# Optimization experiments

Measured on AMD Instinct MI355X. Metric: run time of the kernel, lower is better.

## Reference

```python
import jax, jax.numpy as jnp
import numpy as np

D_MODEL = 1024
NUM_HEADS = 16
D_HEAD = D_MODEL // NUM_HEADS
B, T = 2, 2048


def setup_inputs() -> dict:
    key = jax.random.key(0)
    kx, kq, kk, kv, ko = jax.random.split(key, 5)
    # xavier_uniform bound for square (D,D) linear weights
    bound = float(np.sqrt(6.0 / (D_MODEL + D_MODEL)))
    uni = lambda k: jax.random.uniform(k, (D_MODEL, D_MODEL), jnp.float32, -bound, bound)
    return {
        "x": jax.random.normal(kx, (B, T, D_MODEL), jnp.float32),
        "Wq": uni(kq),
        "Wk": uni(kk),
        "Wv": uni(kv),
        "Wo": uni(ko),
    }


def _split_heads(x):
    # (B, T, D) -> (B, H, T, d_head)
    b, t, _ = x.shape
    return x.reshape(b, t, NUM_HEADS, D_HEAD).transpose(0, 2, 1, 3)


def _exclusive_output_mod(Y, V):
    dt = V.dtype
    tiny = jnp.asarray(jnp.finfo(dt).tiny, dt)
    eps = jnp.asarray(jnp.finfo(dt).eps, dt)
    v_sq = jnp.sum(V * V, axis=-1, keepdims=True)
    y_dot_v = jnp.sum(Y * V, axis=-1, keepdims=True)
    scale = jnp.where(v_sq > 0, y_dot_v / jnp.maximum(v_sq, tiny), jnp.zeros_like(y_dot_v))
    Z = Y - scale * V
    residual_norm = jnp.linalg.norm(Z, axis=-1, keepdims=True)
    reference_norm = jnp.maximum(
        jnp.linalg.norm(Y, axis=-1, keepdims=True),
        jnp.linalg.norm(V, axis=-1, keepdims=True),
    )
    cleanup_tol = eps * Z.shape[-1] * reference_norm
    return jnp.where((v_sq > 0) & (residual_norm <= cleanup_tol), jnp.zeros_like(Z), Z)


def reference(x, Wq, Wk, Wv, Wo):
    Q = _split_heads(x @ Wq.T)  # (B,H,T,dh)
    K = _split_heads(x @ Wk.T)
    V = _split_heads(x @ Wv.T)
    sm_scale = 1.0 / np.sqrt(D_HEAD)
    scores = jnp.einsum("bhqd,bhkd->bhqk", Q, K) * sm_scale
    P = jax.nn.softmax(scores, axis=-1)
    Y = jnp.einsum("bhqk,bhkd->bhqd", P, V)
    Z = _exclusive_output_mod(Y, V)
    # merge heads: (B,H,T,dh) -> (B,T,D)
    Zm = Z.transpose(0, 2, 1, 3).reshape(x.shape[0], x.shape[1], D_MODEL)
    return Zm @ Wo.T
```

## Files before the change

### kernel.cpp

```cpp
#include <hip/hip_runtime.h>
#include <math.h>

#define DM   1024
#define TTOK 2048
#define NTOK 4096

typedef __bf16 bf16x8 __attribute__((ext_vector_type(8)));
typedef __bf16 bf16x4 __attribute__((ext_vector_type(4)));
typedef float  f32x4  __attribute__((ext_vector_type(4)));
typedef float  f32x16 __attribute__((ext_vector_type(16)));

#define QSCALE 0.18033688011112042f

#if defined(__has_builtin)
#if __has_builtin(__builtin_amdgcn_exp2f)
#define EXP2F(x) __builtin_amdgcn_exp2f(x)
#endif
#endif
#ifndef EXP2F
#define EXP2F(x) exp2f(x)
#endif

#define GLDS16(g, l) __builtin_amdgcn_global_load_lds( \
    (__attribute__((address_space(1))) void*)(g),      \
    (__attribute__((address_space(3))) void*)(l), 16, 0, 0)

__global__ __launch_bounds__(256)
void cvt_all(const float* __restrict__ x,  const float* __restrict__ Wq,
             const float* __restrict__ Wk, const float* __restrict__ Wv,
             const float* __restrict__ Wo, __bf16* __restrict__ dst) {
    size_t g = ((size_t)blockIdx.x * 256 + threadIdx.x) * 8;
    const float* s;
    size_t off;
    const size_t NX = (size_t)NTOK * DM;
    if (g < NX) { s = x; off = g; }
    else {
        size_t gg = g - NX;
        int w = (int)(gg >> 20);
        off = gg & ((1u << 20) - 1);
        s = (w == 0) ? Wq : (w == 1) ? Wk : (w == 2) ? Wv : Wo;
    }
    float4 a = *(const float4*)(s + off);
    float4 b = *(const float4*)(s + off + 4);
    bf16x8 v;
    v[0] = (__bf16)a.x; v[1] = (__bf16)a.y; v[2] = (__bf16)a.z; v[3] = (__bf16)a.w;
    v[4] = (__bf16)b.x; v[5] = (__bf16)b.y; v[6] = (__bf16)b.z; v[7] = (__bf16)b.w;
    *(bf16x8*)(dst + g) = v;
}

#define LSTR 136
#define DBUF 8192

template<int MODE>
__global__ __launch_bounds__(256)
void gemm_bf16(const __bf16* __restrict__ X,
               const __bf16* __restrict__ W0, const __bf16* __restrict__ W1,
               const __bf16* __restrict__ W2,
               __bf16* __restrict__ Oq, __bf16* __restrict__ Ok,
               __bf16* __restrict__ Ovt, float* __restrict__ Of)
{
    const int z = (MODE == 0) ? blockIdx.z : 3;
    const __bf16 *A, *B;
    int m0, n0;
    if (MODE == 0 && z < 2) {
        A = z ? W1 : W0; B = X;
        m0 = blockIdx.y * 128; n0 = blockIdx.x * 128;
    } else if (MODE == 0) {
        A = X; B = W2;
        m0 = blockIdx.x * 128; n0 = blockIdx.y * 128;
    } else {
        A = X; B = W0;
        int f = blockIdx.x + 8 * blockIdx.y;
        int c = f & 7, i = f >> 3;
        m0 = (4 * c + (i & 3)) * 128;
        n0 = (i >> 2) * 128;
    }

    __shared__ __attribute__((aligned(16))) __bf16 smem[128 * LSTR];

    const int tid  = threadIdx.x;
    const int lane = tid & 63;
    const int wave = tid >> 6;
    const int wm = wave & 1, wn = wave >> 1;
    const int col = lane & 15, quad = lane >> 4;

    const __bf16* Ag = A + (size_t)(m0 + (tid >> 2)) * DM + (tid & 3) * 8;
    const __bf16* Bg = B + (size_t)(n0 + (tid >> 2)) * DM + (tid & 3) * 8;
    __bf16* lA = smem + tid * 8;
    __bf16* lB = smem + 4096 + tid * 8;

    f32x4 acc[4][4];
#pragma unroll
    for (int i = 0; i < 4; ++i)
#pragma unroll
        for (int j = 0; j < 4; ++j)
#pragma unroll
            for (int r = 0; r < 4; ++r) acc[i][j][r] = 0.0f;

    GLDS16(Ag,                   lA);
    GLDS16(Ag + (size_t)64 * DM, lA + 2048);
    GLDS16(Bg,                   lB);
    GLDS16(Bg + (size_t)64 * DM, lB + 2048);
    __syncthreads();

    const int nk = DM / 32;
    for (int t = 0; t < nk; ++t) {
        const int cur = (t & 1) * DBUF;
        const int nxt = DBUF - cur;

        if (t + 1 < nk) {
            const int k1 = (t + 1) * 32;
            GLDS16(Ag + k1,                   lA + nxt);
            GLDS16(Ag + (size_t)64 * DM + k1, lA + nxt + 2048);
            GLDS16(Bg + k1,                   lB + nxt);
            GLDS16(Bg + (size_t)64 * DM + k1, lB + nxt + 2048);
        }

        const __bf16* Asr = smem + cur;
        const __bf16* Bsr = smem + cur + 4096;
        bf16x8 af[4], bfr[4];
#pragma unroll
        for (int i = 0; i < 4; ++i)
            af[i] = *(const bf16x8*)&Asr[(wm * 64 + i * 16 + col) * 32 + quad * 8];
#pragma unroll
        for (int j = 0; j < 4; ++j)
            bfr[j] = *(const bf16x8*)&Bsr[(wn * 64 + j * 16 + col) * 32 + quad * 8];
#pragma unroll
        for (int i = 0; i < 4; ++i)
#pragma unroll
            for (int j = 0; j < 4; ++j)
                acc[i][j] = __builtin_amdgcn_mfma_f32_16x16x32_bf16(af[i], bfr[j], acc[i][j], 0, 0, 0);

        __syncthreads();
    }

    if (MODE == 1) {
#pragma unroll
        for (int i = 0; i < 4; ++i)
#pragma unroll
            for (int j = 0; j < 4; ++j) {
                const int mb = m0 + wm * 64 + i * 16 + quad * 4;
                const int n  = n0 + wn * 64 + j * 16 + col;
#pragma unroll
                for (int r = 0; r < 4; ++r)
                    Of[(size_t)(mb + r) * DM + n] = acc[i][j][r];
            }
        return;
    }

    const float sc = (z == 0) ? QSCALE : 1.0f;
#pragma unroll
    for (int i = 0; i < 4; ++i)
#pragma unroll
        for (int j = 0; j < 4; ++j) {
            const int ml = wm * 64 + i * 16 + quad * 4;
            const int nl = wn * 64 + j * 16 + col;
            bf16x4 pk;
#pragma unroll
            for (int r = 0; r < 4; ++r) pk[r] = (__bf16)(acc[i][j][r] * sc);
            *(bf16x4*)&smem[nl * LSTR + ml] = pk;
        }
    __syncthreads();

#pragma unroll
    for (int it = 0; it < 8; ++it) {
        int c   = tid + 256 * it;
        int row = c >> 4;
        int ch  = (c & 15) * 8;
        bf16x8 v = *(const bf16x8*)&smem[row * LSTR + ch];
        if (z < 2) {
            int t  = n0 + row;
            int b  = t >> 11; t &= 2047;
            int hd = m0 + ch;
            int h  = hd >> 6, d = hd & 63;
            *(bf16x8*)&((z ? Ok : Oq)[(((size_t)(b * 16 + h)) * TTOK + t) * 64 + d]) = v;
        } else {
            int hd = n0 + row;
            int h  = hd >> 6, d = hd & 63;
            int t  = m0 + ch;
            int b  = t >> 11; t &= 2047;
            *(bf16x8*)&Ovt[(((size_t)(b * 16 + h)) * 64 + d) * TTOK + t] = v;
        }
    }
}

__global__ __launch_bounds__(256)
void attn_mfma(const __bf16* __restrict__ Qg, const __bf16* __restrict__ Kg,
               const __bf16* __restrict__ Vtg, __bf16* __restrict__ Zm)
{
    const int bh = blockIdx.y;
    const int q0 = blockIdx.x * 128;
    const size_t base = (size_t)bh * TTOK * 64;

    __shared__ __attribute__((aligned(16))) __bf16 Ks[2][64 * 72];
    __shared__ __attribute__((aligned(16))) __bf16 Vs[2][64 * 72];
    __shared__ __attribute__((aligned(16))) __bf16 Ps[128 * 72];

    const int tid  = threadIdx.x;
    const int lane = tid & 63, wave = tid >> 6;
    const int c32  = lane & 31, h32 = lane >> 5;

    bf16x8 qf[4];
    const __bf16* qrow = Qg + base + (size_t)(q0 + wave * 32 + c32) * 64 + h32 * 8;
#pragma unroll
    for (int st = 0; st < 4; ++st)
        qf[st] = *(const bf16x8*)(qrow + st * 16);

    f32x16 O[2];
#pragma unroll
    for (int r = 0; r < 16; ++r) { O[0][r] = 0.0f; O[1][r] = 0.0f; }
    float lsum = 0.0f;

    const int rs = tid >> 2, soff = (tid & 3) * 16;

    bf16x8 kr0 = *(const bf16x8*)(Kg  + base + (size_t)rs * 64 + soff);
    bf16x8 kr1 = *(const bf16x8*)(Kg  + base + (size_t)rs * 64 + soff + 8);
    bf16x8 vr0 = *(const bf16x8*)(Vtg + base + (size_t)rs * TTOK + soff);
    bf16x8 vr1 = *(const bf16x8*)(Vtg + base + (size_t)rs * TTOK + soff + 8);
    *(bf16x8*)&Ks[0][rs * 72 + soff]     = kr0;
    *(bf16x8*)&Ks[0][rs * 72 + soff + 8] = kr1;
    *(bf16x8*)&Vs[0][rs * 72 + soff]     = vr0;
    *(bf16x8*)&Vs[0][rs * 72 + soff + 8] = vr1;
    {
        const __bf16* kp = Kg  + base + (size_t)(64 + rs) * 64 + soff;
        const __bf16* vp = Vtg + base + (size_t)rs * TTOK + 64 + soff;
        kr0 = *(const bf16x8*)(kp); kr1 = *(const bf16x8*)(kp + 8);
        vr0 = *(const bf16x8*)(vp); vr1 = *(const bf16x8*)(vp + 8);
    }
    __syncthreads();

    const int kb_tgt = (q0 >> 6) + (wave >> 1);
    const int qo     = (wave & 1) * 32 + c32;
    float vq[2][16];

    for (int kb = 0; kb < TTOK / 64; ++kb) {
        const int cur = kb & 1;
        const __bf16* Kc = Ks[cur];
        const __bf16* Vc = Vs[cur];

        f32x16 s0, s1;
#pragma unroll
        for (int r = 0; r < 16; ++r) { s0[r] = 0.0f; s1[r] = 0.0f; }
#pragma unroll
        for (int st = 0; st < 4; ++st) {
            bf16x8 a0 = *(const bf16x8*)&Kc[(c32)      * 72 + h32 * 8 + st * 16];
            bf16x8 a1 = *(const bf16x8*)&Kc[(32 + c32) * 72 + h32 * 8 + st * 16];
            s0 = __builtin_amdgcn_mfma_f32_32x32x16_bf16(a0, qf[st], s0, 0, 0, 0);
            s1 = __builtin_amdgcn_mfma_f32_32x32x16_bf16(a1, qf[st], s1, 0, 0, 0);
        }

#pragma unroll
        for (int kb2 = 0; kb2 < 2; ++kb2) {
#pragma unroll
            for (int g = 0; g < 4; ++g) {
                float p0 = EXP2F(kb2 ? s1[4 * g + 0] : s0[4 * g + 0]);
                float p1 = EXP2F(kb2 ? s1[4 * g + 1] : s0[4 * g + 1]);
                float p2 = EXP2F(kb2 ? s1[4 * g + 2] : s0[4 * g + 2]);
                float p3 = EXP2F(kb2 ? s1[4 * g + 3] : s0[4 * g + 3]);
                lsum += (p0 + p1) + (p2 + p3);
                bf16x4 pk;
                pk[0] = (__bf16)p0; pk[1] = (__bf16)p1;
                pk[2] = (__bf16)p2; pk[3] = (__bf16)p3;
                *(bf16x4*)&Ps[(wave * 32 + c32) * 72 + kb2 * 32 + g * 8 + h32 * 4] = pk;
            }
        }

#pragma unroll
        for (int ks = 0; ks < 4; ++ks) {
            bf16x8 pf = *(const bf16x8*)&Ps[(wave * 32 + c32) * 72 + h32 * 8 + ks * 16];
            bf16x8 v0 = *(const bf16x8*)&Vc[(c32)      * 72 + h32 * 8 + ks * 16];
            bf16x8 v1 = *(const bf16x8*)&Vc[(32 + c32) * 72 + h32 * 8 + ks * 16];
            O[0] = __builtin_amdgcn_mfma_f32_32x32x16_bf16(v0, pf, O[0], 0, 0, 0);
            O[1] = __builtin_amdgcn_mfma_f32_32x32x16_bf16(v1, pf, O[1], 0, 0, 0);
        }

        if (kb == kb_tgt) {
#pragma unroll
            for (int db = 0; db < 2; ++db)
#pragma unroll
                for (int rg = 0; rg < 16; ++rg) {
                    int d = db * 32 + (rg & 3) + 8 * (rg >> 2) + 4 * h32;
                    vq[db][rg] = (float)Vc[d * 72 + qo];
                }
        }

        __bf16* Kn = Ks[cur ^ 1];
        __bf16* Vn = Vs[cur ^ 1];
        *(bf16x8*)&Kn[rs * 72 + soff]     = kr0;
        *(bf16x8*)&Kn[rs * 72 + soff + 8] = kr1;
        *(bf16x8*)&Vn[rs * 72 + soff]     = vr0;
        *(bf16x8*)&Vn[rs * 72 + soff + 8] = vr1;

        {
            int kbn = (kb + 2) & (TTOK / 64 - 1);
            const __bf16* kp = Kg  + base + (size_t)(kbn * 64 + rs) * 64 + soff;
            const __bf16* vp = Vtg + base + (size_t)rs * TTOK + kbn * 64 + soff;
            kr0 = *(const bf16x8*)(kp); kr1 = *(const bf16x8*)(kp + 8);
            vr0 = *(const bf16x8*)(vp); vr1 = *(const bf16x8*)(vp + 8);
        }

        __syncthreads();
    }

    const float ltot = lsum + __shfl_xor(lsum, 32, 64);
    const float inv  = 1.0f / ltot;

    const int b = bh >> 4, h = bh & 15;
    const int q = q0 + wave * 32 + c32;
    float y[2][16];
    float yv = 0.f, v2 = 0.f, yy = 0.f;
#pragma unroll
    for (int db = 0; db < 2; ++db)
#pragma unroll
        for (int rg = 0; rg < 16; ++rg) {
            float yval = O[db][rg] * inv;
            float vval = vq[db][rg];
            y[db][rg] = yval;
            yv += yval * vval; v2 += vval * vval; yy += yval * yval;
        }
    yv += __shfl_xor(yv, 32, 64);
    v2 += __shfl_xor(v2, 32, 64);
    yy += __shfl_xor(yy, 32, 64);
    float scl = (v2 > 0.0f) ? yv / fmaxf(v2, 1.1754943508222875e-38f) : 0.0f;
    float zz = 0.f;
    float zvv[2][16];
#pragma unroll
    for (int db = 0; db < 2; ++db)
#pragma unroll
        for (int rg = 0; rg < 16; ++rg) {
            zvv[db][rg] = y[db][rg] - scl * vq[db][rg];
            zz += zvv[db][rg] * zvv[db][rg];
        }
    zz += __shfl_xor(zz, 32, 64);
    float znorm = sqrtf(zz);
    float refn  = fmaxf(sqrtf(yy), sqrtf(v2));
    bool  wipe  = (v2 > 0.0f) && (znorm <= 1.1920928955078125e-07f * 64.0f * refn);
#pragma unroll
    for (int db = 0; db < 2; ++db)
#pragma unroll
        for (int g = 0; g < 4; ++g) {
            bf16x4 pk;
#pragma unroll
            for (int r = 0; r < 4; ++r)
                pk[r] = (__bf16)(wipe ? 0.0f : zvv[db][4 * g + r]);
            int d = db * 32 + 8 * g + 4 * h32;
            *(bf16x4*)&Zm[((size_t)(b * TTOK + q)) * DM + h * 64 + d] = pk;
        }
}

extern "C" void kernel_launch(void* const* d_in, const int* in_sizes, int n_in,
                              void* d_out, int out_size, void* d_ws, size_t ws_size,
                              hipStream_t stream) {
    const float* x  = (const float*)d_in[0];
    const float* Wq = (const float*)d_in[1];
    const float* Wk = (const float*)d_in[2];
    const float* Wv = (const float*)d_in[3];
    const float* Wo = (const float*)d_in[4];

    const size_t NX = (size_t)NTOK * DM;
    const size_t NW = (size_t)DM * DM;
    __bf16* xb  = (__bf16*)d_ws;
    __bf16* wqb = xb  + NX;
    __bf16* wkb = wqb + NW;
    __bf16* wvb = wkb + NW;
    __bf16* wob = wvb + NW;
    __bf16* Qb  = wob + NW;
    __bf16* Kb  = Qb  + NX;
    __bf16* Vtb = Kb  + NX;
    __bf16* Zmb = Vtb + NX;

    cvt_all<<<(NX + 4 * NW) / 2048, 256, 0, stream>>>(x, Wq, Wk, Wv, Wo, xb);

    gemm_bf16<0><<<dim3(32, 8, 3), 256, 0, stream>>>(
        xb, wqb, wkb, wvb, Qb, Kb, Vtb, nullptr);

    attn_mfma<<<dim3(TTOK / 128, 32), 256, 0, stream>>>(Qb, Kb, Vtb, Zmb);

    gemm_bf16<1><<<dim3(8, 32), 256, 0, stream>>>(
        Zmb, wob, nullptr, nullptr, nullptr, nullptr, nullptr, (float*)d_out);
}
```

Baseline: 188.1 us.

## Keep softmax probabilities in registers via lane shuffles; retile output projection

Measured after the change: 185.7 us. Within noise of the previous version (-1.3%).

```diff
diff --git a/kernel.cpp b/kernel.cpp
--- a/kernel.cpp
+++ b/kernel.cpp
@@ -7,6 +7,7 @@
 
 typedef __bf16 bf16x8 __attribute__((ext_vector_type(8)));
 typedef __bf16 bf16x4 __attribute__((ext_vector_type(4)));
+typedef __bf16 bf16x2 __attribute__((ext_vector_type(2)));
 typedef float  f32x4  __attribute__((ext_vector_type(4)));
 typedef float  f32x16 __attribute__((ext_vector_type(16)));
 
@@ -24,6 +25,12 @@
 #define GLDS16(g, l) __builtin_amdgcn_global_load_lds( \
     (__attribute__((address_space(1))) void*)(g),      \
     (__attribute__((address_space(3))) void*)(l), 16, 0, 0)
+
+__device__ __forceinline__ unsigned pk2(float a, float b) {
+    bf16x2 t; t[0] = (__bf16)a; t[1] = (__bf16)b;
+    return __builtin_bit_cast(unsigned, t);
+}
+union FU { unsigned u[4]; bf16x8 v; };
 
 __global__ __launch_bounds__(256)
 void cvt_all(const float* __restrict__ x,  const float* __restrict__ Wq,
@@ -51,29 +58,22 @@
 #define LSTR 136
 #define DBUF 8192
 
-template<int MODE>
 __global__ __launch_bounds__(256)
-void gemm_bf16(const __bf16* __restrict__ X,
-               const __bf16* __restrict__ W0, const __bf16* __restrict__ W1,
-               const __bf16* __restrict__ W2,
-               __bf16* __restrict__ Oq, __bf16* __restrict__ Ok,
-               __bf16* __restrict__ Ovt, float* __restrict__ Of)
+void gemm_qkv(const __bf16* __restrict__ X,
+              const __bf16* __restrict__ W0, const __bf16* __restrict__ W1,
+              const __bf16* __restrict__ W2,
+              __bf16* __restrict__ Oq, __bf16* __restrict__ Ok,
+              __bf16* __restrict__ Ovt)
 {
-    const int z = (MODE == 0) ? blockIdx.z : 3;
+    const int z = blockIdx.z;
     const __bf16 *A, *B;
     int m0, n0;
-    if (MODE == 0 && z < 2) {
+    if (z < 2) {
         A = z ? W1 : W0; B = X;
         m0 = blockIdx.y * 128; n0 = blockIdx.x * 128;
-    } else if (MODE == 0) {
+    } else {
         A = X; B = W2;
         m0 = blockIdx.x * 128; n0 = blockIdx.y * 128;
-    } else {
-        A = X; B = W0;
-        int f = blockIdx.x + 8 * blockIdx.y;
-        int c = f & 7, i = f >> 3;
-        m0 = (4 * c + (i & 3)) * 128;
-        n0 = (i >> 2) * 128;
     }
 
     __shared__ __attribute__((aligned(16))) __bf16 smem[128 * LSTR];
@@ -132,20 +132,6 @@
                 acc[i][j] = __builtin_amdgcn_mfma_f32_16x16x32_bf16(af[i], bfr[j], acc[i][j], 0, 0, 0);
 
         __syncthreads();
-    }
-
-    if (MODE == 1) {
-#pragma unroll
-        for (int i = 0; i < 4; ++i)
-#pragma unroll
-            for (int j = 0; j < 4; ++j) {
-                const int mb = m0 + wm * 64 + i * 16 + quad * 4;
-                const int n  = n0 + wn * 64 + j * 16 + col;
-#pragma unroll
-                for (int r = 0; r < 4; ++r)
-                    Of[(size_t)(mb + r) * DM + n] = acc[i][j][r];
-            }
-        return;
     }
 
     const float sc = (z == 0) ? QSCALE : 1.0f;
@@ -184,6 +170,81 @@
     }
 }
 
+#define ODBUF 6144
+
+__global__ __launch_bounds__(256)
+void gemm_oproj(const __bf16* __restrict__ X, const __bf16* __restrict__ Wo,
+                float* __restrict__ Of)
+{
+    const int f = blockIdx.x + 8 * blockIdx.y;
+    const int c = f & 7, i0 = f >> 3;
+    const int m0 = (8 * c + (i0 & 7)) * 64;
+    const int n0 = (i0 >> 3) * 128;
+
+    __shared__ __attribute__((aligned(16))) __bf16 smem[2 * ODBUF];
+
+    const int tid  = threadIdx.x;
+    const int lane = tid & 63;
+    const int wave = tid >> 6;
+    const int col = lane & 15, quad = lane >> 4;
+
+    const __bf16* Ag = X  + (size_t)(m0 + (tid >> 2)) * DM + (tid & 3) * 8;
+    const __bf16* Bg = Wo + (size_t)(n0 + (tid >> 2)) * DM + (tid & 3) * 8;
+    __bf16* lA = smem + tid * 8;
+    __bf16* lB = smem + 2048 + tid * 8;
+
+    f32x4 acc[4][2];
+#pragma unroll
+    for (int i = 0; i < 4; ++i)
+#pragma unroll
+        for (int j = 0; j < 2; ++j)
+#pragma unroll
+            for (int r = 0; r < 4; ++r) acc[i][j][r] = 0.0f;
+
+    GLDS16(Ag,                   lA);
+    GLDS16(Bg,                   lB);
+    GLDS16(Bg + (size_t)64 * DM, lB + 2048);
+    __syncthreads();
+
+    const int nk = DM / 32;
+    for (int t = 0; t < nk; ++t) {
+        const int cur = (t & 1) * ODBUF;
+        const int nxt = ODBUF - cur;
+        if (t + 1 < nk) {
+            const int k1 = (t + 1) * 32;
+            GLDS16(Ag + k1,                   lA + nxt);
+            GLDS16(Bg + k1,                   lB + nxt);
+            GLDS16(Bg + (size_t)64 * DM + k1, lB + nxt + 2048);
+        }
+        const __bf16* Asr = smem + cur;
+        const __bf16* Bsr = smem + cur + 2048;
+        bf16x8 af[4], bfr[2];
+#pragma unroll
+        for (int i = 0; i < 4; ++i)
+            af[i] = *(const bf16x8*)&Asr[(i * 16 + col) * 32 + quad * 8];
+#pragma unroll
+        for (int j = 0; j < 2; ++j)
+            bfr[j] = *(const bf16x8*)&Bsr[(wave * 32 + j * 16 + col) * 32 + quad * 8];
+#pragma unroll
+        for (int i = 0; i < 4; ++i)
+#pragma unroll
+            for (int j = 0; j < 2; ++j)
+                acc[i][j] = __builtin_amdgcn_mfma_f32_16x16x32_bf16(af[i], bfr[j], acc[i][j], 0, 0, 0);
+        __syncthreads();
+    }
+
+#pragma unroll
+    for (int i = 0; i < 4; ++i)
+#pragma unroll
+        for (int j = 0; j < 2; ++j) {
+            const int mb = m0 + i * 16 + quad * 4;
+            const int n  = n0 + wave * 32 + j * 16 + col;
+#pragma unroll
+            for (int r = 0; r < 4; ++r)
+                Of[(size_t)(mb + r) * DM + n] = acc[i][j][r];
+        }
+}
+
 __global__ __launch_bounds__(256)
 void attn_mfma(const __bf16* __restrict__ Qg, const __bf16* __restrict__ Kg,
                const __bf16* __restrict__ Vtg, __bf16* __restrict__ Zm)
@@ -194,7 +255,6 @@
 
     __shared__ __attribute__((aligned(16))) __bf16 Ks[2][64 * 72];
     __shared__ __attribute__((aligned(16))) __bf16 Vs[2][64 * 72];
-    __shared__ __attribute__((aligned(16))) __bf16 Ps[128 * 72];
 
     const int tid  = threadIdx.x;
     const int lane = tid & 63, wave = tid >> 6;
@@ -249,29 +309,39 @@
             s1 = __builtin_amdgcn_mfma_f32_32x32x16_bf16(a1, qf[st], s1, 0, 0, 0);
         }
 
-#pragma unroll
-        for (int kb2 = 0; kb2 < 2; ++kb2) {
-#pragma unroll
-            for (int g = 0; g < 4; ++g) {
-                float p0 = EXP2F(kb2 ? s1[4 * g + 0] : s0[4 * g + 0]);
-                float p1 = EXP2F(kb2 ? s1[4 * g + 1] : s0[4 * g + 1]);
-                float p2 = EXP2F(kb2 ? s1[4 * g + 2] : s0[4 * g + 2]);
-                float p3 = EXP2F(kb2 ? s1[4 * g + 3] : s0[4 * g + 3]);
-                lsum += (p0 + p1) + (p2 + p3);
-                bf16x4 pk;
-                pk[0] = (__bf16)p0; pk[1] = (__bf16)p1;
-                pk[2] = (__bf16)p2; pk[3] = (__bf16)p3;
-                *(bf16x4*)&Ps[(wave * 32 + c32) * 72 + kb2 * 32 + g * 8 + h32 * 4] = pk;
-            }
-        }
-
+        float pl0[16], pl1[16];
+#pragma unroll
+        for (int r = 0; r < 16; ++r) { pl0[r] = EXP2F(s0[r]); pl1[r] = EXP2F(s1[r]); }
+#pragma unroll
+        for (int r = 0; r < 16; ++r) lsum += pl0[r] + pl1[r];
+
+        bf16x8 pf[4];
 #pragma unroll
         for (int ks = 0; ks < 4; ++ks) {
-            bf16x8 pf = *(const bf16x8*)&Ps[(wave * 32 + c32) * 72 + h32 * 8 + ks * 16];
+            const float* pl = (ks & 2) ? pl1 : pl0;
+            const int rb = (ks & 1) * 8;
+            unsigned A0 = pk2(pl[rb + 0], pl[rb + 1]);
+            unsigned A1 = pk2(pl[rb + 2], pl[rb + 3]);
+            unsigned B0 = pk2(pl[rb + 4], pl[rb + 5]);
+            unsigned B1 = pk2(pl[rb + 6], pl[rb + 7]);
+            unsigned s0w = h32 ? A0 : B0;
+            unsigned s1w = h32 ? A1 : B1;
+            unsigned r0 = __shfl_xor(s0w, 32, 64);
+            unsigned r1 = __shfl_xor(s1w, 32, 64);
+            FU fu;
+            fu.u[0] = h32 ? r0 : A0;
+            fu.u[1] = h32 ? r1 : A1;
+            fu.u[2] = h32 ? B0 : r0;
+            fu.u[3] = h32 ? B1 : r1;
+            pf[ks] = fu.v;
+        }
+
+#pragma unroll
+        for (int ks = 0; ks < 4; ++ks) {
             bf16x8 v0 = *(const bf16x8*)&Vc[(c32)      * 72 + h32 * 8 + ks * 16];
             bf16x8 v1 = *(const bf16x8*)&Vc[(32 + c32) * 72 + h32 * 8 + ks * 16];
-            O[0] = __builtin_amdgcn_mfma_f32_32x32x16_bf16(v0, pf, O[0], 0, 0, 0);
-            O[1] = __builtin_amdgcn_mfma_f32_32x32x16_bf16(v1, pf, O[1], 0, 0, 0);
+            O[0] = __builtin_amdgcn_mfma_f32_32x32x16_bf16(v0, pf[ks], O[0], 0, 0, 0);
+            O[1] = __builtin_amdgcn_mfma_f32_32x32x16_bf16(v1, pf[ks], O[1], 0, 0, 0);
         }
 
         if (kb == kb_tgt) {
@@ -371,11 +441,10 @@
 
     cvt_all<<<(NX + 4 * NW) / 2048, 256, 0, stream>>>(x, Wq, Wk, Wv, Wo, xb);
 
-    gemm_bf16<0><<<dim3(32, 8, 3), 256, 0, stream>>>(
-        xb, wqb, wkb, wvb, Qb, Kb, Vtb, nullptr);
+    gemm_qkv<<<dim3(32, 8, 3), 256, 0, stream>>>(
+        xb, wqb, wkb, wvb, Qb, Kb, Vtb);
 
     attn_mfma<<<dim3(TTOK / 128, 32), 256, 0, stream>>>(Qb, Kb, Vtb, Zmb);
 
-    gemm_bf16<1><<<dim3(8, 32), 256, 0, stream>>>(
-        Zmb, wob, nullptr, nullptr, nullptr, nullptr, nullptr, (float*)d_out);
-}
+    gemm_oproj<<<dim3(8, 64), 256, 0, stream>>>(Zmb, wob, (float*)d_out);
+}
```
